# Performance work log

Measured on AMD Instinct MI355X. Metric: run time of the kernel, lower is better.

## Reference

```python
import jax, jax.numpy as jnp
import numpy as np

N, N_SPINS, N_HIDDEN = 8192, 1024, 1024


def setup_inputs() -> dict:
    key = jax.random.key(0)
    ks = jax.random.split(key, 6)
    s_in = 1.0 / np.sqrt(N_SPINS)
    s_h = 1.0 / np.sqrt(N_HIDDEN)
    return {
        "x": jax.random.normal(ks[0], (N, N_SPINS), dtype=jnp.float32),
        "W_in": jax.random.normal(ks[1], (N_HIDDEN, N_SPINS), dtype=jnp.float32) * s_in,
        "b_in": jax.random.normal(ks[2], (N_HIDDEN,), dtype=jnp.float32) * s_in,
        "Wq": jax.random.normal(ks[3], (N_HIDDEN, N_HIDDEN), dtype=jnp.float32) * s_h,
        "Wk": jax.random.normal(ks[4], (N_HIDDEN, N_HIDDEN), dtype=jnp.float32) * s_h,
        "Wv": jax.random.normal(ks[5], (N_HIDDEN, N_HIDDEN), dtype=jnp.float32) * s_h,
    }


def reference(x, W_in, b_in, Wq, Wk, Wv):
    # embedding: Linear(n_spins, n_hidden)  -> h: [N, H]
    h = x @ W_in.T + b_in
    q = h @ Wq.T                      # [N, H]
    k = h @ Wk.T                      # [N, H]
    v = h @ Wv.T                      # [N, H]
    scores = (q @ k.T) * 0.25         # [N, N], scale 1/4 as in source
    attn = jax.nn.softmax(scores, axis=0)  # softmax over dim=0 (columns)
    out = attn @ v                    # [N, H]
    # log(cosh(z)) = |z| + log1p(exp(-2|z|)) - log(2), numerically stable
    a = jnp.abs(out)
    logcosh = a + jnp.log1p(jnp.exp(-2.0 * a)) - jnp.log(jnp.asarray(2.0, out.dtype))
    return jnp.sum(logcosh, axis=-1)  # [N]
```

## Files before the change

kernel.cpp:

```cpp
#include <hip/hip_runtime.h>
#include <hip/hip_bf16.h>
#include <cstdint>
#include <cstddef>

#define NTOK 8192
#define NHID 1024

typedef __attribute__((ext_vector_type(8))) __bf16 bf16x8;
typedef __attribute__((ext_vector_type(4))) float f32x4;

__device__ __forceinline__ unsigned short f2bf(float f) {
    union { float f; unsigned u; } v; v.f = f;
    unsigned r = v.u + 0x7FFF + ((v.u >> 16) & 1);
    return (unsigned short)(r >> 16);
}

__device__ __forceinline__ float bf2f(unsigned short u) {
    union { unsigned u; float f; } v; v.u = ((unsigned)u) << 16;
    return v.f;
}

__device__ __forceinline__ void async_copy16(const void* gsrc, void* ldsdst) {
    __builtin_amdgcn_global_load_lds(
        (const __attribute__((address_space(1))) unsigned int*)gsrc,
        (__attribute__((address_space(3))) unsigned int*)ldsdst,
        16, 0, 0);
}

template <int EPI, bool SWAP>
__global__ __launch_bounds__(512, 2) void gemm_bt3(
    const unsigned short* __restrict__ A,
    const unsigned short* __restrict__ B,
    void* __restrict__ C,
    const float* __restrict__ bias,
    float* __restrict__ zsum,
    float scale, int M, int N, int K, int lda, int ldb)
{
    __shared__ __attribute__((aligned(16))) unsigned short lds[3][24576];

    const int tid  = threadIdx.x;
    const int wave = tid >> 6;
    const int lane = tid & 63;
    const int bm = (SWAP ? blockIdx.x : blockIdx.y) * 256;
    const int bn = (SWAP ? blockIdx.y : blockIdx.x) * 128;
    const size_t ldaz = (size_t)lda;
    const size_t ldbz = (size_t)ldb;

    const int srow = lane >> 3;
    const int scol = ((lane & 7) ^ srow) * 8;
    const unsigned short* Ag[4];
    const unsigned short* Bg[2];
    int Aoff[4], Boff[2];
#pragma unroll
    for (int t = 0; t < 4; ++t) {
        int r = (wave * 4 + t) * 8 + srow;
        Ag[t] = A + (size_t)(bm + r) * ldaz + scol;
        Aoff[t] = (wave * 4 + t) * 512;
    }
#pragma unroll
    for (int t = 0; t < 2; ++t) {
        int r = (wave * 2 + t) * 8 + srow;
        Bg[t] = B + (size_t)(bn + r) * ldbz + scol;
        Boff[t] = 16384 + (wave * 2 + t) * 512;
    }

    const int wm = (wave >> 1) * 64;
    const int wn = (wave & 1) * 64;
    const int fr = lane & 15;
    const int frl = fr & 7;
    const int q = lane >> 4;

    f32x4 acc[4][4] = {};

    const int nt = K >> 6;

    {
        unsigned short* b0 = &lds[0][0];
        unsigned short* b1 = &lds[1][0];
#pragma unroll
        for (int u = 0; u < 4; ++u) { async_copy16(Ag[u], b0 + Aoff[u]); Ag[u] += 64; }
#pragma unroll
        for (int u = 0; u < 2; ++u) { async_copy16(Bg[u], b0 + Boff[u]); Bg[u] += 64; }
#pragma unroll
        for (int u = 0; u < 4; ++u) { async_copy16(Ag[u], b1 + Aoff[u]); Ag[u] += 64; }
#pragma unroll
        for (int u = 0; u < 2; ++u) { async_copy16(Bg[u], b1 + Boff[u]); Bg[u] += 64; }
        asm volatile("s_waitcnt vmcnt(6)" ::: "memory");
        __builtin_amdgcn_s_barrier();
    }

    int cb = 0;
    int sb = 2;
    for (int t = 0; t < nt; ++t) {
        const unsigned short* As = &lds[cb][0];
        const unsigned short* Bs = &lds[cb][16384];
        unsigned short* Sb = &lds[sb][0];
        const bool pf = (t + 2 < nt);

        {
            const int pc = (q ^ frl) * 8;
            bf16x8 a[4], b[4];
#pragma unroll
            for (int i = 0; i < 4; ++i) {
                a[i] = *(const bf16x8*)&As[(wm + i * 16 + fr) * 64 + pc];
                b[i] = *(const bf16x8*)&Bs[(wn + i * 16 + fr) * 64 + pc];
            }
            if (pf) {
#pragma unroll
                for (int u = 0; u < 4; ++u) { async_copy16(Ag[u], Sb + Aoff[u]); Ag[u] += 64; }
            }
            __builtin_amdgcn_s_barrier();
            asm volatile("s_waitcnt lgkmcnt(0)" ::: "memory");
            __builtin_amdgcn_s_setprio(1);
#pragma unroll
            for (int i = 0; i < 4; ++i)
#pragma unroll
                for (int j = 0; j < 4; ++j)
                    acc[i][j] = __builtin_amdgcn_mfma_f32_16x16x32_bf16(
                        a[i], b[j], acc[i][j], 0, 0, 0);
            __builtin_amdgcn_s_setprio(0);
            __builtin_amdgcn_s_barrier();
        }

        {
            const int pc = ((4 + q) ^ frl) * 8;
            bf16x8 a[4], b[4];
#pragma unroll
            for (int i = 0; i < 4; ++i) {
                a[i] = *(const bf16x8*)&As[(wm + i * 16 + fr) * 64 + pc];
                b[i] = *(const bf16x8*)&Bs[(wn + i * 16 + fr) * 64 + pc];
            }
            if (pf) {
#pragma unroll
                for (int u = 0; u < 2; ++u) { async_copy16(Bg[u], Sb + Boff[u]); Bg[u] += 64; }
            }
            __builtin_amdgcn_s_barrier();
            asm volatile("s_waitcnt lgkmcnt(0)" ::: "memory");
            __builtin_amdgcn_s_setprio(1);
#pragma unroll
            for (int i = 0; i < 4; ++i)
#pragma unroll
                for (int j = 0; j < 4; ++j)
                    acc[i][j] = __builtin_amdgcn_mfma_f32_16x16x32_bf16(
                        a[i], b[j], acc[i][j], 0, 0, 0);
            __builtin_amdgcn_s_setprio(0);
            if (t < nt - 2)       asm volatile("s_waitcnt vmcnt(6)" ::: "memory");
            else if (t == nt - 2) asm volatile("s_waitcnt vmcnt(0)" ::: "memory");
            __builtin_amdgcn_s_barrier();
        }

        if (pf) sb = (sb == 2) ? 0 : sb + 1;
        cb = (cb == 2) ? 0 : cb + 1;
    }

    const int erow = q * 4;
#pragma unroll
    for (int j = 0; j < 4; ++j) {
        const int gcol = bn + wn + j * 16 + fr;
        const float bv = (EPI == 1 && bias) ? bias[gcol] : 0.0f;
        float colsum = 0.0f;
#pragma unroll
        for (int i = 0; i < 4; ++i) {
            const int grow0 = bm + wm + i * 16 + erow;
#pragma unroll
            for (int r = 0; r < 4; ++r) {
                float v;
                if (EPI == 2) {
                    v = __expf(fmaf(acc[i][j][r], scale, -64.0f));
                    colsum += v;
                } else {
                    v = acc[i][j][r] * scale + bv;
                }
                size_t idx = (size_t)(grow0 + r) * N + gcol;
                if (EPI == 0) ((float*)C)[idx] = v;
                else          ((unsigned short*)C)[idx] = f2bf(v);
            }
        }
        if (EPI == 2) {
            colsum += __shfl_xor(colsum, 16, 64);
            colsum += __shfl_xor(colsum, 32, 64);
            if (q == 0) atomicAdd(&zsum[gcol], colsum);
        }
    }
}

__global__ void cvt_all(const float4* __restrict__ x,
                        const float4* __restrict__ w0,
                        const float4* __restrict__ w1,
                        const float4* __restrict__ w2,
                        const float4* __restrict__ w3,
                        ushort4* __restrict__ xb,
                        ushort4* __restrict__ wdst,
                        float4* __restrict__ pz4,
                        int n4x, int n4w)
{
    int i = blockIdx.x * blockDim.x + threadIdx.x;
    int n4 = n4x + 4 * n4w;
    if (i >= n4) {
        int zi = i - n4;
        if (zi < 2048) pz4[zi] = make_float4(0.f, 0.f, 0.f, 0.f);
        return;
    }
    float4 f;
    ushort4* dst;
    if (i < n4x) {
        f = x[i]; dst = xb + i;
    } else {
        int r = i - n4x;
        int seg = r / n4w, off = r % n4w;
        const float4* src = (seg == 0) ? w0 : (seg == 1) ? w1 : (seg == 2) ? w2 : w3;
        f = src[off]; dst = wdst + r;
    }
    ushort4 o;
    o.x = f2bf(f.x); o.y = f2bf(f.y); o.z = f2bf(f.z); o.w = f2bf(f.w);
    *dst = o;
}

__global__ __launch_bounds__(256) void transpose_scale(
    const unsigned short* __restrict__ v,
    const float* __restrict__ z,
    unsigned short* __restrict__ vt)
{
    __shared__ float lds[64 * 65];
    const int tid = threadIdx.x;
    const int j0 = blockIdx.x * 64;
    const int h0 = blockIdx.y * 64;
    const int c = tid & 63;
    const int r0 = tid >> 6;
#pragma unroll
    for (int it = 0; it < 16; ++it) {
        int r = it * 4 + r0;
        lds[r * 65 + c] = bf2f(v[(size_t)(j0 + r) * 3072 + h0 + c]);
    }
    __syncthreads();
    const float rz = 1.0f / z[j0 + c];
#pragma unroll
    for (int it = 0; it < 16; ++it) {
        int r = it * 4 + r0;
        vt[(size_t)(h0 + r) * NTOK + j0 + c] = f2bf(lds[c * 65 + r] * rz);
    }
}

__global__ void logcosh_rowsum(const ushort4* __restrict__ O4,
                               float* __restrict__ out)
{
    const float LN2 = 0.69314718055994531f;
    int row = blockIdx.x;
    ushort4 u = O4[(size_t)row * 256 + threadIdx.x];
    float s = 0.0f, a;
    a = fabsf(bf2f(u.x)); s += a + log1pf(__expf(-2.0f * a));
    a = fabsf(bf2f(u.y)); s += a + log1pf(__expf(-2.0f * a));
    a = fabsf(bf2f(u.z)); s += a + log1pf(__expf(-2.0f * a));
    a = fabsf(bf2f(u.w)); s += a + log1pf(__expf(-2.0f * a));
    s -= 4.0f * LN2;
    for (int off = 32; off; off >>= 1) s += __shfl_down(s, off, 64);
    __shared__ float red[4];
    if ((threadIdx.x & 63) == 0) red[threadIdx.x >> 6] = s;
    __syncthreads();
    if (threadIdx.x == 0) out[row] = red[0] + red[1] + red[2] + red[3];
}

extern "C" void kernel_launch(void* const* d_in, const int* in_sizes, int n_in,
                              void* d_out, int out_size, void* d_ws, size_t ws_size,
                              hipStream_t stream)
{
    (void)in_sizes; (void)n_in; (void)out_size; (void)ws_size;

    const float* x    = (const float*)d_in[0];
    const float* W_in = (const float*)d_in[1];
    const float* b_in = (const float*)d_in[2];
    const float* Wq   = (const float*)d_in[3];
    const float* Wk   = (const float*)d_in[4];
    const float* Wv   = (const float*)d_in[5];
    float* out = (float*)d_out;

    char* w = (char*)d_ws;
    const size_t MiB = 1024 * 1024;
    unsigned short* Pb     = (unsigned short*)(w);
    unsigned short* qkv    = (unsigned short*)(w + 128 * MiB);
    unsigned short* xb     = (unsigned short*)(w + 128 * MiB);
    unsigned short* outb   = (unsigned short*)(w + 128 * MiB);
    unsigned short* hb     = (unsigned short*)(w + 176 * MiB);
    unsigned short* vtb    = (unsigned short*)(w + 176 * MiB);
    unsigned short* wib    = (unsigned short*)(w + 192 * MiB);
    unsigned short* wqkvb  = (unsigned short*)(w + 194 * MiB);
    float*          pz     = (float*)         (w + 200 * MiB);

    {
        int n4x = NTOK * NHID / 4;
        int n4w = NHID * NHID / 4;
        int n4  = n4x + 4 * n4w;
        cvt_all<<<n4 / 256 + 8, 256, 0, stream>>>(
            (const float4*)x, (const float4*)W_in, (const float4*)Wq,
            (const float4*)Wk, (const float4*)Wv,
            (ushort4*)xb, (ushort4*)wib, (float4*)pz, n4x, n4w);
    }

    dim3 gNH(NHID / 128, NTOK / 256);
    gemm_bt3<1, false><<<gNH, 512, 0, stream>>>(
        xb, wib, hb, b_in, nullptr, 1.0f, NTOK, NHID, NHID, NHID, NHID);

    dim3 gQKV(3 * NHID / 128, NTOK / 256);
    gemm_bt3<1, false><<<gQKV, 512, 0, stream>>>(
        hb, wqkvb, qkv, nullptr, nullptr, 1.0f, NTOK, 3 * NHID, NHID, NHID, NHID);

    dim3 gS(NTOK / 128, NTOK / 256);
    gemm_bt3<2, false><<<gS, 512, 0, stream>>>(
        qkv, qkv + NHID, Pb, nullptr, pz, 0.25f, NTOK, NTOK, NHID,
        3 * NHID, 3 * NHID);

    dim3 gT(NTOK / 64, NHID / 64);
    transpose_scale<<<gT, 256, 0, stream>>>(qkv + 2 * NHID, pz, vtb);

    dim3 gO(NTOK / 256, NHID / 128);
    gemm_bt3<1, true><<<gO, 512, 0, stream>>>(
        Pb, vtb, outb, nullptr, nullptr, 1.0f, NTOK, NHID, NTOK, NTOK, NTOK);

    logcosh_rowsum<<<NTOK, 256, 0, stream>>>((const ushort4*)outb, out);
}
```

Baseline: 477.4 us.

## Software-pipeline LDS fragment reads against MFMAs in GEMM main loop

Restructures the GEMM inner loop so that LDS fragment loads for the next half-tile, including the first half of the next K-tile, are issued before the current MFMA block runs. This double-buffers register fragments and cuts the number of barriers per iteration from four to two. The aim is to hide LDS latency behind matrix-core work. It raises register pressure and changes the vmcnt wait accounting, which could hurt occupancy or correctness if the wait counts are wrong.

```diff
diff --git a/kernel.cpp b/kernel.cpp
--- a/kernel.cpp
+++ b/kernel.cpp
@@ -28,7 +28,7 @@
 }
 
 template <int EPI, bool SWAP>
-__global__ __launch_bounds__(512, 2) void gemm_bt3(
+__global__ __launch_bounds__(512, 2) void gemm_bt4(
     const unsigned short* __restrict__ A,
     const unsigned short* __restrict__ B,
     void* __restrict__ C,
@@ -70,6 +70,9 @@
     const int frl = fr & 7;
     const int q = lane >> 4;
 
+    const int pc0 = (q ^ frl) * 8;
+    const int pc1 = ((4 + q) ^ frl) * 8;
+
     f32x4 acc[4][4] = {};
 
     const int nt = K >> 6;
@@ -86,72 +89,98 @@
 #pragma unroll
         for (int u = 0; u < 2; ++u) { async_copy16(Bg[u], b1 + Boff[u]); Bg[u] += 64; }
         asm volatile("s_waitcnt vmcnt(6)" ::: "memory");
-        __builtin_amdgcn_s_barrier();
-    }
+        asm volatile("s_barrier" ::: "memory");
+    }
+
+    bf16x8 a0_0, a0_1, a0_2, a0_3, b0_0, b0_1, b0_2, b0_3;
+    bf16x8 a1_0, a1_1, a1_2, a1_3, b1_0, b1_1, b1_2, b1_3;
+
+    {
+        const unsigned short* As = &lds[0][0];
+        const unsigned short* Bs = &lds[0][16384];
+        a0_0 = *(const bf16x8*)&As[(wm +  0 + fr) * 64 + pc0];
+        a0_1 = *(const bf16x8*)&As[(wm + 16 + fr) * 64 + pc0];
+        a0_2 = *(const bf16x8*)&As[(wm + 32 + fr) * 64 + pc0];
+        a0_3 = *(const bf16x8*)&As[(wm + 48 + fr) * 64 + pc0];
+        b0_0 = *(const bf16x8*)&Bs[(wn +  0 + fr) * 64 + pc0];
+        b0_1 = *(const bf16x8*)&Bs[(wn + 16 + fr) * 64 + pc0];
+        b0_2 = *(const bf16x8*)&Bs[(wn + 32 + fr) * 64 + pc0];
+        b0_3 = *(const bf16x8*)&Bs[(wn + 48 + fr) * 64 + pc0];
+    }
+
+#define MFMA16(AA0, AA1, AA2, AA3, BB0, BB1, BB2, BB3)                         \
+    do {                                                                       \
+        __builtin_amdgcn_s_setprio(1);                                         \
+        acc[0][0] = __builtin_amdgcn_mfma_f32_16x16x32_bf16(AA0, BB0, acc[0][0], 0, 0, 0); \
+        acc[0][1] = __builtin_amdgcn_mfma_f32_16x16x32_bf16(AA0, BB1, acc[0][1], 0, 0, 0); \
+        acc[0][2] = __builtin_amdgcn_mfma_f32_16x16x32_bf16(AA0, BB2, acc[0][2], 0, 0, 0); \
+        acc[0][3] = __builtin_amdgcn_mfma_f32_16x16x32_bf16(AA0, BB3, acc[0][3], 0, 0, 0); \
+        acc[1][0] = __builtin_amdgcn_mfma_f32_16x16x32_bf16(AA1, BB0, acc[1][0], 0, 0, 0); \
+        acc[1][1] = __builtin_amdgcn_mfma_f32_16x16x32_bf16(AA1, BB1, acc[1][1], 0, 0, 0); \
+        acc[1][2] = __builtin_amdgcn_mfma_f32_16x16x32_bf16(AA1, BB2, acc[1][2], 0, 0, 0); \
+        acc[1][3] = __builtin_amdgcn_mfma_f32_16x16x32_bf16(AA1, BB3, acc[1][3], 0, 0, 0); \
+        acc[2][0] = __builtin_amdgcn_mfma_f32_16x16x32_bf16(AA2, BB0, acc[2][0], 0, 0, 0); \
+        acc[2][1] = __builtin_amdgcn_mfma_f32_16x16x32_bf16(AA2, BB1, acc[2][1], 0, 0, 0); \
+        acc[2][2] = __builtin_amdgcn_mfma_f32_16x16x32_bf16(AA2, BB2, acc[2][2], 0, 0, 0); \
+        acc[2][3] = __builtin_amdgcn_mfma_f32_16x16x32_bf16(AA2, BB3, acc[2][3], 0, 0, 0); \
+        acc[3][0] = __builtin_amdgcn_mfma_f32_16x16x32_bf16(AA3, BB0, acc[3][0], 0, 0, 0); \
+        acc[3][1] = __builtin_amdgcn_mfma_f32_16x16x32_bf16(AA3, BB1, acc[3][1], 0, 0, 0); \
+        acc[3][2] = __builtin_amdgcn_mfma_f32_16x16x32_bf16(AA3, BB2, acc[3][2], 0, 0, 0); \
+        acc[3][3] = __builtin_amdgcn_mfma_f32_16x16x32_bf16(AA3, BB3, acc[3][3], 0, 0, 0); \
+        __builtin_amdgcn_s_setprio(0);                                         \
+    } while (0)
 
     int cb = 0;
     int sb = 2;
     for (int t = 0; t < nt; ++t) {
+        const bool pf = (t + 2 < nt);
         const unsigned short* As = &lds[cb][0];
         const unsigned short* Bs = &lds[cb][16384];
         unsigned short* Sb = &lds[sb][0];
-        const bool pf = (t + 2 < nt);
-
-        {
-            const int pc = (q ^ frl) * 8;
-            bf16x8 a[4], b[4];
-#pragma unroll
-            for (int i = 0; i < 4; ++i) {
-                a[i] = *(const bf16x8*)&As[(wm + i * 16 + fr) * 64 + pc];
-                b[i] = *(const bf16x8*)&Bs[(wn + i * 16 + fr) * 64 + pc];
-            }
-            if (pf) {
-#pragma unroll
-                for (int u = 0; u < 4; ++u) { async_copy16(Ag[u], Sb + Aoff[u]); Ag[u] += 64; }
-            }
-            __builtin_amdgcn_s_barrier();
-            asm volatile("s_waitcnt lgkmcnt(0)" ::: "memory");
-            __builtin_amdgcn_s_setprio(1);
-#pragma unroll
-            for (int i = 0; i < 4; ++i)
-#pragma unroll
-                for (int j = 0; j < 4; ++j)
-                    acc[i][j] = __builtin_amdgcn_mfma_f32_16x16x32_bf16(
-                        a[i], b[j], acc[i][j], 0, 0, 0);
-            __builtin_amdgcn_s_setprio(0);
-            __builtin_amdgcn_s_barrier();
-        }
-
-        {
-            const int pc = ((4 + q) ^ frl) * 8;
-            bf16x8 a[4], b[4];
-#pragma unroll
-            for (int i = 0; i < 4; ++i) {
-                a[i] = *(const bf16x8*)&As[(wm + i * 16 + fr) * 64 + pc];
-                b[i] = *(const bf16x8*)&Bs[(wn + i * 16 + fr) * 64 + pc];
-            }
-            if (pf) {
-#pragma unroll
-                for (int u = 0; u < 2; ++u) { async_copy16(Bg[u], Sb + Boff[u]); Bg[u] += 64; }
-            }
-            __builtin_amdgcn_s_barrier();
-            asm volatile("s_waitcnt lgkmcnt(0)" ::: "memory");
-            __builtin_amdgcn_s_setprio(1);
-#pragma unroll
-            for (int i = 0; i < 4; ++i)
-#pragma unroll
-                for (int j = 0; j < 4; ++j)
-                    acc[i][j] = __builtin_amdgcn_mfma_f32_16x16x32_bf16(
-                        a[i], b[j], acc[i][j], 0, 0, 0);
-            __builtin_amdgcn_s_setprio(0);
-            if (t < nt - 2)       asm volatile("s_waitcnt vmcnt(6)" ::: "memory");
-            else if (t == nt - 2) asm volatile("s_waitcnt vmcnt(0)" ::: "memory");
-            __builtin_amdgcn_s_barrier();
-        }
+        const int nb = (cb == 2) ? 0 : cb + 1;
+        const unsigned short* An = &lds[nb][0];
+        const unsigned short* Bn = &lds[nb][16384];
+
+        a1_0 = *(const bf16x8*)&As[(wm +  0 + fr) * 64 + pc1];
+        a1_1 = *(const bf16x8*)&As[(wm + 16 + fr) * 64 + pc1];
+        a1_2 = *(const bf16x8*)&As[(wm + 32 + fr) * 64 + pc1];
+        a1_3 = *(const bf16x8*)&As[(wm + 48 + fr) * 64 + pc1];
+        b1_0 = *(const bf16x8*)&Bs[(wn +  0 + fr) * 64 + pc1];
+        b1_1 = *(const bf16x8*)&Bs[(wn + 16 + fr) * 64 + pc1];
+        b1_2 = *(const bf16x8*)&Bs[(wn + 32 + fr) * 64 + pc1];
+        b1_3 = *(const bf16x8*)&Bs[(wn + 48 + fr) * 64 + pc1];
+        if (pf) {
+#pragma unroll
+            for (int u = 0; u < 4; ++u) { async_copy16(Ag[u], Sb + Aoff[u]); Ag[u] += 64; }
+        }
+        __builtin_amdgcn_sched_barrier(0);
+        MFMA16(a0_0, a0_1, a0_2, a0_3, b0_0, b0_1, b0_2, b0_3);
+        if (t < nt - 2) asm volatile("s_waitcnt vmcnt(4)" ::: "memory");
+        else            asm volatile("s_waitcnt vmcnt(0)" ::: "memory");
+        asm volatile("s_barrier" ::: "memory");
+
+        if (t + 1 < nt) {
+            a0_0 = *(const bf16x8*)&An[(wm +  0 + fr) * 64 + pc0];
+            a0_1 = *(const bf16x8*)&An[(wm + 16 + fr) * 64 + pc0];
+            a0_2 = *(const bf16x8*)&An[(wm + 32 + fr) * 64 + pc0];
+            a0_3 = *(const bf16x8*)&An[(wm + 48 + fr) * 64 + pc0];
+            b0_0 = *(const bf16x8*)&Bn[(wn +  0 + fr) * 64 + pc0];
+            b0_1 = *(const bf16x8*)&Bn[(wn + 16 + fr) * 64 + pc0];
+            b0_2 = *(const bf16x8*)&Bn[(wn + 32 + fr) * 64 + pc0];
+            b0_3 = *(const bf16x8*)&Bn[(wn + 48 + fr) * 64 + pc0];
+        }
+        if (pf) {
+#pragma unroll
+            for (int u = 0; u < 2; ++u) { async_copy16(Bg[u], Sb + Boff[u]); Bg[u] += 64; }
+        }
+        __builtin_amdgcn_sched_barrier(0);
+        MFMA16(a1_0, a1_1, a1_2, a1_3, b1_0, b1_1, b1_2, b1_3);
+        asm volatile("s_barrier" ::: "memory");
 
         if (pf) sb = (sb == 2) ? 0 : sb + 1;
-        cb = (cb == 2) ? 0 : cb + 1;
-    }
+        cb = nb;
+    }
+#undef MFMA16
 
     const int erow = q * 4;
 #pragma unroll
@@ -297,15 +326,15 @@
     }
 
     dim3 gNH(NHID / 128, NTOK / 256);
-    gemm_bt3<1, false><<<gNH, 512, 0, stream>>>(
+    gemm_bt4<1, false><<<gNH, 512, 0, stream>>>(
         xb, wib, hb, b_in, nullptr, 1.0f, NTOK, NHID, NHID, NHID, NHID);
 
     dim3 gQKV(3 * NHID / 128, NTOK / 256);
-    gemm_bt3<1, false><<<gQKV, 512, 0, stream>>>(
+    gemm_bt4<1, false><<<gQKV, 512, 0, stream>>>(
         hb, wqkvb, qkv, nullptr, nullptr, 1.0f, NTOK, 3 * NHID, NHID, NHID, NHID);
 
     dim3 gS(NTOK / 128, NTOK / 256);
-    gemm_bt3<2, false><<<gS, 512, 0, stream>>>(
+    gemm_bt4<2, false><<<gS, 512, 0, stream>>>(
         qkv, qkv + NHID, Pb, nullptr, pz, 0.25f, NTOK, NTOK, NHID,
         3 * NHID, 3 * NHID);
 
@@ -313,7 +342,7 @@
     transpose_scale<<<gT, 256, 0, stream>>>(qkv + 2 * NHID, pz, vtb);
 
     dim3 gO(NTOK / 256, NHID / 128);
-    gemm_bt3<1, true><<<gO, 512, 0, stream>>>(
+    gemm_bt4<1, true><<<gO, 512, 0, stream>>>(
         Pb, vtb, outb, nullptr, nullptr, 1.0f, NTOK, NHID, NTOK, NTOK, NTOK);
 
     logcosh_rowsum<<<NTOK, 256, 0, stream>>>((const ushort4*)outb, out);
```

Result: no change. 474.1 us (-0.7%).
